# Kernel tuning notes

Measured on AMD Instinct MI355X. Metric: run time of the kernel, lower is better.

Reference implementation:

```python
import jax, jax.numpy as jnp
import numpy as np

K = 3          # kernel size
KF = K * K     # kernel field = 9
PAD = 1
STRIDE = 1


def _conv(x, w, b):
    y = jax.lax.conv_general_dilated(
        x, w, (STRIDE, STRIDE), [(PAD, PAD), (PAD, PAD)],
        dimension_numbers=('NCHW', 'OIHW', 'NCHW'))
    return y + b[None, :, None, None]


def _bilinear_gather(x, py, px):
    # x: [B,C,H,W]; py/px: [B,KF,Ho,Wo] float sampling coords (zero-pad outside)
    B, C, H, W = x.shape
    xf = x.reshape(B, C, H * W)
    y0 = jnp.floor(py)
    x0 = jnp.floor(px)

    def corner(yc, xc):
        wy = 1.0 - jnp.abs(py - yc)
        wx = 1.0 - jnp.abs(px - xc)
        valid = (yc >= 0) & (yc <= H - 1) & (xc >= 0) & (xc <= W - 1)
        yi = jnp.clip(yc, 0, H - 1).astype(jnp.int32)
        xi = jnp.clip(xc, 0, W - 1).astype(jnp.int32)
        idx = (yi * W + xi).reshape(B, -1)               # [B, KF*Ho*Wo]
        v = jax.vmap(lambda f, i: f[:, i])(xf, idx)      # [B, C, KF*Ho*Wo]
        wgt = (wy * wx * valid.astype(x.dtype)).reshape(B, 1, -1)
        return v * wgt

    return (corner(y0, x0) + corner(y0, x0 + 1) +
            corner(y0 + 1, x0) + corner(y0 + 1, x0 + 1))  # [B,C,KF*Ho*Wo]


def _deform_conv(x, offset, mask, w, b):
    # modulated deformable conv v2 (mmcv offset layout: [y,x] interleaved per kernel pt)
    B, C, H, W = x.shape
    Ho, Wo = mask.shape[2], mask.shape[3]
    kh, kw = jnp.meshgrid(jnp.arange(K), jnp.arange(K), indexing='ij')
    kh = kh.reshape(-1).astype(x.dtype)   # [KF]
    kw = kw.reshape(-1).astype(x.dtype)
    base_y = (jnp.arange(Ho) * STRIDE - PAD).astype(x.dtype)
    base_x = (jnp.arange(Wo) * STRIDE - PAD).astype(x.dtype)
    off = offset.reshape(B, KF, 2, Ho, Wo)
    py = base_y[None, None, :, None] + kh[None, :, None, None] + off[:, :, 0]
    px = base_x[None, None, None, :] + kw[None, :, None, None] + off[:, :, 1]
    val = _bilinear_gather(x, py, px).reshape(B, C, KF, Ho, Wo)
    val = val * mask[:, None]                             # modulate
    out = jnp.einsum('bckhw,ock->bohw', val, w.reshape(w.shape[0], C, KF))
    return out + b[None, :, None, None]


def setup_inputs() -> dict:
    key = jax.random.key(0)
    k1, k2, k3 = jax.random.split(key, 3)
    B, C, H, W = 8, 64, 128, 128
    x = jax.random.normal(k1, (B, C, H, W), dtype=jnp.float32)
    w_om = jax.random.normal(k2, (3 * KF, C, K, K), dtype=jnp.float32) * 0.02
    b_om = jnp.zeros((3 * KF,), dtype=jnp.float32)
    w_dc = jax.random.normal(k3, (64, C, K, K), dtype=jnp.float32) * 0.05
    b_dc = jnp.zeros((64,), dtype=jnp.float32)
    return {"x": x, "w_om": w_om, "b_om": b_om, "w_dc": w_dc, "b_dc": b_dc}


def reference(x, w_om, b_om, w_dc, b_dc):
    om = _conv(x, w_om, b_om)                 # [B, 3*KF, H, W]
    offset = om[:, :2 * KF]
    mask = 2.0 * jax.nn.sigmoid(om[:, 2 * KF:])
    return _deform_conv(x, offset, mask, w_dc, b_dc)
```

## Files before the change

### kernel.cpp

```cpp
#include <hip/hip_runtime.h>
#include <cmath>

#define IH 128
#define IW 128
#define NB 8

typedef __attribute__((ext_vector_type(8))) short bf16x8;
typedef __attribute__((ext_vector_type(4))) float f32x4;
typedef __attribute__((ext_vector_type(2))) float f32x2;

union U4B8 { uint4 u; bf16x8 h; };

#define OFFM_OFF 0
#define XT_OFF   3538944
#define WTDC_OFF (3538944 + 4194304)
#define WTOM_OFF (3538944 + 4194304 + 18432)

__device__ __forceinline__ unsigned short f32_to_bf16(float f) {
    unsigned int u = __float_as_uint(f);
    u += 0x7fffu + ((u >> 16) & 1u);
    return (unsigned short)(u >> 16);
}

__global__ void transpose_weights(const float* __restrict__ w_dc,
                                  const float* __restrict__ w_om,
                                  unsigned short* __restrict__ wt_dc16,
                                  unsigned short* __restrict__ wt_om16) {
    int idx = blockIdx.x * blockDim.x + threadIdx.x;
    if (idx < 9 * 64 * 64) {
        int k = idx >> 12;
        int o = (idx >> 6) & 63;
        int c = idx & 63;
        wt_dc16[idx] = f32_to_bf16(w_dc[(o * 64 + c) * 9 + k]);
    }
    if (idx < 9 * 32 * 64) {
        int k = idx >> 11;
        int o = (idx >> 6) & 31;
        int c = idx & 63;
        wt_om16[idx] = (o < 27) ? f32_to_bf16(w_om[(o * 64 + c) * 9 + k])
                                : (unsigned short)0;
    }
}

__global__ __launch_bounds__(256) void transpose_x(
        const float* __restrict__ x, unsigned short* __restrict__ xT) {
    __shared__ float t[64 * 65];
    const int tid = threadIdx.x;
    const int blk = blockIdx.x;
    const int b = blk >> 8;
    const int rem = blk & 255;
    const int h = rem >> 1;
    const int w0 = (rem & 1) << 6;

    for (int i = tid; i < 4096; i += 256) {
        const int c = i >> 6;
        const int w = i & 63;
        t[w * 65 + c] = x[(((size_t)(b * 64 + c)) << 14) + (h << 7) + w0 + w];
    }
    __syncthreads();
    const int c2 = (tid & 31) * 2;
    ushort2* dst = (ushort2*)(xT + (((size_t)b << 20)) + ((size_t)((h << 7) + w0)) * 64 + c2);
#pragma unroll
    for (int p = 0; p < 8; ++p) {
        const int w = (tid >> 5) + p * 8;
        ushort2 u;
        u.x = f32_to_bf16(t[w * 65 + c2]);
        u.y = f32_to_bf16(t[w * 65 + c2 + 1]);
        dst[(size_t)w * 32] = u;
    }
}

__device__ __forceinline__ void issue_gather(
        const unsigned short* __restrict__ xb, const float* offs,
        int k, int lpx, int h, int w0, int quad, uint4* g, float* cw) {
    const float offy = offs[(k << 1) * 65 + lpx];
    const float offx = offs[((k << 1) + 1) * 65 + lpx];
    const float msk  = offs[(18 + k) * 65 + lpx];
    const int kh = k / 3;
    const int kw = k - kh * 3;
    const float py  = (float)(h + kh - 1) + offy;
    const float pxf = (float)(w0 + lpx + kw - 1) + offx;
    const float y0f = floorf(py);
    const float x0f = floorf(pxf);
    const float fy = py - y0f;
    const float fx = pxf - x0f;
    const float wy0 = 1.0f - fy, wx0 = 1.0f - fx;
    const float vy0 = (y0f >= 0.0f && y0f <= 127.0f) ? 1.0f : 0.0f;
    const float vy1 = (y0f >= -1.0f && y0f <= 126.0f) ? 1.0f : 0.0f;
    const float vx0 = (x0f >= 0.0f && x0f <= 127.0f) ? 1.0f : 0.0f;
    const float vx1 = (x0f >= -1.0f && x0f <= 126.0f) ? 1.0f : 0.0f;
    cw[0] = wy0 * wx0 * vy0 * vx0 * msk;
    cw[1] = wy0 * fx  * vy0 * vx1 * msk;
    cw[2] = fy  * wx0 * vy1 * vx0 * msk;
    cw[3] = fy  * fx  * vy1 * vx1 * msk;
    const int y0i = min(max((int)y0f, 0), 127);
    const int y1i = min(max((int)y0f + 1, 0), 127);
    const int x0i = min(max((int)x0f, 0), 127);
    const int x1i = min(max((int)x0f + 1, 0), 127);
    const int cofs = quad << 3;
    const unsigned short* p00 = xb + ((((size_t)((y0i << 7) + x0i)) << 6) + cofs);
    const unsigned short* p01 = xb + ((((size_t)((y0i << 7) + x1i)) << 6) + cofs);
    const unsigned short* p10 = xb + ((((size_t)((y1i << 7) + x0i)) << 6) + cofs);
    const unsigned short* p11 = xb + ((((size_t)((y1i << 7) + x1i)) << 6) + cofs);
    g[0] = *(const uint4*)p00;  g[1] = *(const uint4*)(p00 + 32);
    g[2] = *(const uint4*)p01;  g[3] = *(const uint4*)(p01 + 32);
    g[4] = *(const uint4*)p10;  g[5] = *(const uint4*)(p10 + 32);
    g[6] = *(const uint4*)p11;  g[7] = *(const uint4*)(p11 + 32);
}

__device__ __forceinline__ void pack_frags(const uint4* g, const float* cw,
                                           U4B8& a0, U4B8& a1) {
    f32x2 v2[8];
#pragma unroll
    for (int i = 0; i < 8; ++i) v2[i] = (f32x2){0.f, 0.f};
#pragma unroll
    for (int c = 0; c < 4; ++c) {
        f32x2 w2;
        w2.x = cw[c];
        w2.y = cw[c];
        const uint4 ga = g[2 * c];
        const uint4 gb = g[2 * c + 1];
        const unsigned int u[8] = {ga.x, ga.y, ga.z, ga.w, gb.x, gb.y, gb.z, gb.w};
#pragma unroll
        for (int i = 0; i < 8; ++i) {
            f32x2 x2;
            x2.x = __uint_as_float(u[i] << 16);
            x2.y = __uint_as_float(u[i] & 0xffff0000u);
            asm("v_pk_fma_f32 %0, %1, %2, %0" : "+v"(v2[i]) : "v"(x2), "v"(w2));
        }
    }
    unsigned int pk[8];
#pragma unroll
    for (int i = 0; i < 8; ++i)
        asm("v_cvt_pk_bf16_f32 %0, %1, %2"
            : "=v"(pk[i]) : "v"(v2[i].x), "v"(v2[i].y));
    a0.u = make_uint4(pk[0], pk[1], pk[2], pk[3]);
    a1.u = make_uint4(pk[4], pk[5], pk[6], pk[7]);
}

__global__ __launch_bounds__(256) void om_deform_fused(
        const unsigned short* __restrict__ xT,
        const float* __restrict__ b_om,
        const unsigned short* __restrict__ wt_om16,
        const float* __restrict__ b_dc,
        const unsigned short* __restrict__ wt_dc16,
        float* __restrict__ out) {
    __shared__ __align__(16) float offs[27 * 65];
    __shared__ __align__(16) unsigned short wks[2][64 * 72];

    const int tid = threadIdx.x;
    const int bid = blockIdx.x;
    const int swz = ((bid & 7) << 8) + (bid >> 3);
    const int b = swz >> 8;
    const int rem = swz & 255;
    const int h = rem >> 1;
    const int w0 = (rem & 1) << 6;
    const int wid = tid >> 6;
    const int lane = tid & 63;
    const int ln15 = lane & 15;
    const int quad = lane >> 4;
    const int lpx = (wid << 4) + ln15;

    const unsigned short* xb = xT + ((size_t)b << 20);

    f32x4 oacc[2] = {{0.f, 0.f, 0.f, 0.f}, {0.f, 0.f, 0.f, 0.f}};
    uint4 pa[2][2];
    int   pav[2];
    uint4 pb[2][4];

#define ISSUE_A(K, S)                                                         \
    {                                                                         \
        const int kh_ = (K) / 3, kw_ = (K) - kh_ * 3;                         \
        const int y_ = h + kh_ - 1;                                           \
        const int xg_ = w0 + lpx + kw_ - 1;                                   \
        pav[S] = (y_ >= 0 && y_ < IH && xg_ >= 0 && xg_ < IW);                \
        const int yc_ = min(max(y_, 0), IH - 1);                              \
        const int xc_ = min(max(xg_, 0), IW - 1);                             \
        const unsigned short* p_ =                                            \
            xb + ((((size_t)((yc_ << 7) + xc_)) << 6) + (quad << 3));         \
        pa[S][0] = *(const uint4*)p_;                                         \
        pa[S][1] = *(const uint4*)(p_ + 32);                                  \
    }
#define ISSUE_B(K, S)                                                         \
    {                                                                         \
        const unsigned short* wg_ = wt_om16 + ((K) << 11) + (quad << 3);      \
        const unsigned short* q0_ = wg_ + (ln15 << 6);                        \
        const unsigned short* q1_ = wg_ + ((16 + ln15) << 6);                 \
        pb[S][0] = *(const uint4*)q0_;                                        \
        pb[S][1] = *(const uint4*)(q0_ + 32);                                 \
        pb[S][2] = *(const uint4*)q1_;                                        \
        pb[S][3] = *(const uint4*)(q1_ + 32);                                 \
    }

    ISSUE_B(0, 0)
    ISSUE_A(0, 0)
#pragma unroll
    for (int k = 0; k < 9; ++k) {
        const int cur = k & 1;
        const int nxt = cur ^ 1;
        if (k < 8) {
            ISSUE_B(k + 1, nxt)
            ISSUE_A(k + 1, nxt)
        }
        const uint4 z = make_uint4(0u, 0u, 0u, 0u);
        U4B8 a0, a1, b00, b01, b10, b11;
        a0.u = pav[cur] ? pa[cur][0] : z;
        a1.u = pav[cur] ? pa[cur][1] : z;
        b00.u = pb[cur][0];
        b01.u = pb[cur][1];
        b10.u = pb[cur][2];
        b11.u = pb[cur][3];
        oacc[0] = __builtin_amdgcn_mfma_f32_16x16x32_bf16(a0.h, b00.h, oacc[0], 0, 0, 0);
        oacc[0] = __builtin_amdgcn_mfma_f32_16x16x32_bf16(a1.h, b01.h, oacc[0], 0, 0, 0);
        oacc[1] = __builtin_amdgcn_mfma_f32_16x16x32_bf16(a0.h, b10.h, oacc[1], 0, 0, 0);
        oacc[1] = __builtin_amdgcn_mfma_f32_16x16x32_bf16(a1.h, b11.h, oacc[1], 0, 0, 0);
    }
#undef ISSUE_A
#undef ISSUE_B

    const int so0 = tid >> 3, sp = tid & 7;
    const int so1 = so0 + 32;
    {
        const uint4 wv0 = *(const uint4*)(wt_dc16 + (so0 << 6) + (sp << 3));
        const uint4 wv1 = *(const uint4*)(wt_dc16 + (so1 << 6) + (sp << 3));
        *(uint4*)&wks[0][so0 * 72 + sp * 8] = wv0;
        *(uint4*)&wks[0][so1 * 72 + sp * 8] = wv1;
    }

    const int px0 = (wid << 4) + (quad << 2);
#pragma unroll
    for (int ot = 0; ot < 2; ++ot) {
        const int o = (ot << 4) + ln15;
        if (o < 27) {
            const float bias = b_om[o];
            float r[4];
            r[0] = oacc[ot][0] + bias;
            r[1] = oacc[ot][1] + bias;
            r[2] = oacc[ot][2] + bias;
            r[3] = oacc[ot][3] + bias;
            if (o >= 18) {
#pragma unroll
                for (int j = 0; j < 4; ++j)
                    r[j] = 2.0f / (1.0f + __expf(-r[j]));
            }
#pragma unroll
            for (int j = 0; j < 4; ++j)
                offs[o * 65 + px0 + j] = r[j];
        }
    }
    __syncthreads();

    f32x4 acc[4];
#pragma unroll
    for (int i = 0; i < 4; ++i) acc[i] = (f32x4){0.f, 0.f, 0.f, 0.f};

    uint4 g[2][8];
    float cw[2][4];
    issue_gather(xb, offs, 0, lpx, h, w0, quad, g[0], cw[0]);

#pragma unroll
    for (int k = 0; k < 9; ++k) {
        const int cur = k & 1;
        const int nxt = cur ^ 1;
        if (k < 8) {
            const uint4 wv0 = *(const uint4*)(wt_dc16 + ((k + 1) << 12) + (so0 << 6) + (sp << 3));
            const uint4 wv1 = *(const uint4*)(wt_dc16 + ((k + 1) << 12) + (so1 << 6) + (sp << 3));
            issue_gather(xb, offs, k + 1, lpx, h, w0, quad, g[nxt], cw[nxt]);
            *(uint4*)&wks[nxt][so0 * 72 + sp * 8] = wv0;
            *(uint4*)&wks[nxt][so1 * 72 + sp * 8] = wv1;
        }
        U4B8 a0, a1;
        pack_frags(g[cur], cw[cur], a0, a1);
        const unsigned short* wb = wks[cur];
#pragma unroll
        for (int ot = 0; ot < 4; ++ot) {
            U4B8 b0, b1;
            const unsigned short* base = &wb[((ot << 4) + ln15) * 72 + (quad << 3)];
            b0.u = *(const uint4*)base;
            b1.u = *(const uint4*)(base + 32);
            acc[ot] = __builtin_amdgcn_mfma_f32_16x16x32_bf16(a0.h, b0.h, acc[ot], 0, 0, 0);
            acc[ot] = __builtin_amdgcn_mfma_f32_16x16x32_bf16(a1.h, b1.h, acc[ot], 0, 0, 0);
        }
        if (k < 8) {
            asm volatile("s_waitcnt lgkmcnt(0)" ::: "memory");
            __builtin_amdgcn_s_barrier();
            __builtin_amdgcn_sched_barrier(0);
        }
    }

#pragma unroll
    for (int ot = 0; ot < 4; ++ot) {
        const int o = (ot << 4) + ln15;
        const float bias = b_dc[o];
        float4 r;
        r.x = acc[ot][0] + bias;
        r.y = acc[ot][1] + bias;
        r.z = acc[ot][2] + bias;
        r.w = acc[ot][3] + bias;
        *(float4*)&out[(((size_t)(b * 64 + o)) << 14) + (h << 7) + w0 + (wid << 4) + (quad << 2)] = r;
    }
}

extern "C" void kernel_launch(void* const* d_in, const int* in_sizes, int n_in,
                              void* d_out, int out_size, void* d_ws, size_t ws_size,
                              hipStream_t stream) {
    const float* x    = (const float*)d_in[0];
    const float* w_om = (const float*)d_in[1];
    const float* b_om = (const float*)d_in[2];
    const float* w_dc = (const float*)d_in[3];
    const float* b_dc = (const float*)d_in[4];
    float* out = (float*)d_out;
    float* ws  = (float*)d_ws;

    unsigned short* xT      = (unsigned short*)(ws + XT_OFF);
    unsigned short* wt_dc16 = (unsigned short*)(ws + WTDC_OFF);
    unsigned short* wt_om16 = (unsigned short*)(ws + WTOM_OFF);

    const int n_blocks = NB * IH * (IW / 64);

    transpose_weights<<<144, 256, 0, stream>>>(w_dc, w_om, wt_dc16, wt_om16);
    transpose_x<<<NB * IH * 2, 256, 0, stream>>>(x, xT);
    om_deform_fused<<<n_blocks, 256, 0, stream>>>(xT, b_om, wt_om16, b_dc, wt_dc16, out);
}
```

Measured before the change: 202.7 us.

## Stage offset-conv input window in LDS and vectorize x transpose

The offset/mask convolution now loads a 3x66 pixel halo window of the transposed input into shared memory once. Its nine kernel taps then read from LDS instead of issuing separate global loads per tap. The LDS window shares space with the later offset and weight buffers through a union, which costs an extra barrier. Separately, the x transpose kernel now handles a full row per block, using float4 loads and packed bf16 conversion with 16-byte stores, to cut global memory transactions.

```diff
diff --git a/kernel.cpp b/kernel.cpp
--- a/kernel.cpp
+++ b/kernel.cpp
@@ -44,29 +44,35 @@
 
 __global__ __launch_bounds__(256) void transpose_x(
         const float* __restrict__ x, unsigned short* __restrict__ xT) {
-    __shared__ float t[64 * 65];
+    __shared__ __align__(16) float t[64][132];
     const int tid = threadIdx.x;
-    const int blk = blockIdx.x;
-    const int b = blk >> 8;
-    const int rem = blk & 255;
-    const int h = rem >> 1;
-    const int w0 = (rem & 1) << 6;
-
-    for (int i = tid; i < 4096; i += 256) {
-        const int c = i >> 6;
-        const int w = i & 63;
-        t[w * 65 + c] = x[(((size_t)(b * 64 + c)) << 14) + (h << 7) + w0 + w];
+    const int b = blockIdx.x >> 7;
+    const int h = blockIdx.x & 127;
+
+#pragma unroll
+    for (int j = 0; j < 8; ++j) {
+        const int i = (j << 8) + tid;
+        const int c = i >> 5;
+        const int w4 = i & 31;
+        const float4 v = *(const float4*)&x[(((size_t)(b * 64 + c)) << 14) + (h << 7) + (w4 << 2)];
+        *(float4*)&t[c][w4 << 2] = v;
     }
     __syncthreads();
-    const int c2 = (tid & 31) * 2;
-    ushort2* dst = (ushort2*)(xT + (((size_t)b << 20)) + ((size_t)((h << 7) + w0)) * 64 + c2);
-#pragma unroll
-    for (int p = 0; p < 8; ++p) {
-        const int w = (tid >> 5) + p * 8;
-        ushort2 u;
-        u.x = f32_to_bf16(t[w * 65 + c2]);
-        u.y = f32_to_bf16(t[w * 65 + c2 + 1]);
-        dst[(size_t)w * 32] = u;
+
+#pragma unroll
+    for (int j = 0; j < 4; ++j) {
+        const int u = (j << 8) + tid;
+        const int px = u & 127;
+        const int cg = u >> 7;
+        unsigned int pk[4];
+#pragma unroll
+        for (int e = 0; e < 4; ++e) {
+            const float lo = t[(cg << 3) + 2 * e][px];
+            const float hi = t[(cg << 3) + 2 * e + 1][px];
+            asm("v_cvt_pk_bf16_f32 %0, %1, %2" : "=v"(pk[e]) : "v"(lo), "v"(hi));
+        }
+        *(uint4*)(xT + (((size_t)b << 20) + ((size_t)((h << 7) + px) << 6) + (cg << 3))) =
+            make_uint4(pk[0], pk[1], pk[2], pk[3]);
     }
 }
 
@@ -138,6 +144,15 @@
     a1.u = make_uint4(pk[4], pk[5], pk[6], pk[7]);
 }
 
+struct P2Mem {
+    float offs[27 * 65];
+    unsigned short wks[2][64 * 72];
+};
+union SMem {
+    unsigned short win[198 * 72];
+    P2Mem p2;
+};
+
 __global__ __launch_bounds__(256) void om_deform_fused(
         const unsigned short* __restrict__ xT,
         const float* __restrict__ b_om,
@@ -145,8 +160,7 @@
         const float* __restrict__ b_dc,
         const unsigned short* __restrict__ wt_dc16,
         float* __restrict__ out) {
-    __shared__ __align__(16) float offs[27 * 65];
-    __shared__ __align__(16) unsigned short wks[2][64 * 72];
+    __shared__ __align__(16) SMem sm;
 
     const int tid = threadIdx.x;
     const int bid = blockIdx.x;
@@ -163,24 +177,23 @@
 
     const unsigned short* xb = xT + ((size_t)b << 20);
 
+    for (int idx = tid; idx < 1584; idx += 256) {
+        const int pos = idx >> 3;
+        const int part = idx & 7;
+        const int r = pos / 66;
+        const int xx = pos - r * 66;
+        const int y = h + r - 1;
+        const int xg = w0 + xx - 1;
+        uint4 v = make_uint4(0u, 0u, 0u, 0u);
+        if (y >= 0 && y < IH && xg >= 0 && xg < IW)
+            v = *(const uint4*)(xT + (((size_t)b << 20) + (((y << 7) + xg) << 6) + (part << 3)));
+        *(uint4*)&sm.win[pos * 72 + part * 8] = v;
+    }
+    __syncthreads();
+
     f32x4 oacc[2] = {{0.f, 0.f, 0.f, 0.f}, {0.f, 0.f, 0.f, 0.f}};
-    uint4 pa[2][2];
-    int   pav[2];
     uint4 pb[2][4];
 
-#define ISSUE_A(K, S)                                                         \
-    {                                                                         \
-        const int kh_ = (K) / 3, kw_ = (K) - kh_ * 3;                         \
-        const int y_ = h + kh_ - 1;                                           \
-        const int xg_ = w0 + lpx + kw_ - 1;                                   \
-        pav[S] = (y_ >= 0 && y_ < IH && xg_ >= 0 && xg_ < IW);                \
-        const int yc_ = min(max(y_, 0), IH - 1);                              \
-        const int xc_ = min(max(xg_, 0), IW - 1);                             \
-        const unsigned short* p_ =                                            \
-            xb + ((((size_t)((yc_ << 7) + xc_)) << 6) + (quad << 3));         \
-        pa[S][0] = *(const uint4*)p_;                                         \
-        pa[S][1] = *(const uint4*)(p_ + 32);                                  \
-    }
 #define ISSUE_B(K, S)                                                         \
     {                                                                         \
         const unsigned short* wg_ = wt_om16 + ((K) << 11) + (quad << 3);      \
@@ -193,19 +206,17 @@
     }
 
     ISSUE_B(0, 0)
-    ISSUE_A(0, 0)
 #pragma unroll
     for (int k = 0; k < 9; ++k) {
         const int cur = k & 1;
         const int nxt = cur ^ 1;
-        if (k < 8) {
-            ISSUE_B(k + 1, nxt)
-            ISSUE_A(k + 1, nxt)
-        }
-        const uint4 z = make_uint4(0u, 0u, 0u, 0u);
+        if (k < 8) ISSUE_B(k + 1, nxt)
+        const int kh = k / 3;
+        const int kw = k - kh * 3;
+        const int posb = kh * 66 + lpx + kw;
         U4B8 a0, a1, b00, b01, b10, b11;
-        a0.u = pav[cur] ? pa[cur][0] : z;
-        a1.u = pav[cur] ? pa[cur][1] : z;
+        a0.u = *(const uint4*)&sm.win[posb * 72 + (quad << 3)];
+        a1.u = *(const uint4*)&sm.win[posb * 72 + 32 + (quad << 3)];
         b00.u = pb[cur][0];
         b01.u = pb[cur][1];
         b10.u = pb[cur][2];
@@ -215,16 +226,17 @@
         oacc[1] = __builtin_amdgcn_mfma_f32_16x16x32_bf16(a0.h, b10.h, oacc[1], 0, 0, 0);
         oacc[1] = __builtin_amdgcn_mfma_f32_16x16x32_bf16(a1.h, b11.h, oacc[1], 0, 0, 0);
     }
-#undef ISSUE_A
 #undef ISSUE_B
+
+    __syncthreads();
 
     const int so0 = tid >> 3, sp = tid & 7;
     const int so1 = so0 + 32;
     {
         const uint4 wv0 = *(const uint4*)(wt_dc16 + (so0 << 6) + (sp << 3));
         const uint4 wv1 = *(const uint4*)(wt_dc16 + (so1 << 6) + (sp << 3));
-        *(uint4*)&wks[0][so0 * 72 + sp * 8] = wv0;
-        *(uint4*)&wks[0][so1 * 72 + sp * 8] = wv1;
+        *(uint4*)&sm.p2.wks[0][so0 * 72 + sp * 8] = wv0;
+        *(uint4*)&sm.p2.wks[0][so1 * 72 + sp * 8] = wv1;
     }
 
     const int px0 = (wid << 4) + (quad << 2);
@@ -245,7 +257,7 @@
             }
 #pragma unroll
             for (int j = 0; j < 4; ++j)
-                offs[o * 65 + px0 + j] = r[j];
+                sm.p2.offs[o * 65 + px0 + j] = r[j];
         }
     }
     __syncthreads();
@@ -256,7 +268,7 @@
 
     uint4 g[2][8];
     float cw[2][4];
-    issue_gather(xb, offs, 0, lpx, h, w0, quad, g[0], cw[0]);
+    issue_gather(xb, sm.p2.offs, 0, lpx, h, w0, quad, g[0], cw[0]);
 
 #pragma unroll
     for (int k = 0; k < 9; ++k) {
@@ -265,13 +277,13 @@
         if (k < 8) {
             const uint4 wv0 = *(const uint4*)(wt_dc16 + ((k + 1) << 12) + (so0 << 6) + (sp << 3));
             const uint4 wv1 = *(const uint4*)(wt_dc16 + ((k + 1) << 12) + (so1 << 6) + (sp << 3));
-            issue_gather(xb, offs, k + 1, lpx, h, w0, quad, g[nxt], cw[nxt]);
-            *(uint4*)&wks[nxt][so0 * 72 + sp * 8] = wv0;
-            *(uint4*)&wks[nxt][so1 * 72 + sp * 8] = wv1;
+            issue_gather(xb, sm.p2.offs, k + 1, lpx, h, w0, quad, g[nxt], cw[nxt]);
+            *(uint4*)&sm.p2.wks[nxt][so0 * 72 + sp * 8] = wv0;
+            *(uint4*)&sm.p2.wks[nxt][so1 * 72 + sp * 8] = wv1;
         }
         U4B8 a0, a1;
         pack_frags(g[cur], cw[cur], a0, a1);
-        const unsigned short* wb = wks[cur];
+        const unsigned short* wb = sm.p2.wks[cur];
 #pragma unroll
         for (int ot = 0; ot < 4; ++ot) {
             U4B8 b0, b1;
@@ -319,6 +331,6 @@
     const int n_blocks = NB * IH * (IW / 64);
 
     transpose_weights<<<144, 256, 0, stream>>>(w_dc, w_om, wt_dc16, wt_om16);
-    transpose_x<<<NB * IH * 2, 256, 0, stream>>>(x, xT);
+    transpose_x<<<NB * IH, 256, 0, stream>>>(x, xT);
     om_deform_fused<<<n_blocks, 256, 0, stream>>>(xT, b_om, wt_om16, b_dc, wt_dc16, out);
 }
```

Result: no change. 206.0 us (+1.6%).
